# Kernel tuning notes

Hardware: AMD Instinct MI355X
Metric: run time of the kernel (lower is better)

## Reference

```python
import jax, jax.numpy as jnp
import numpy as np

D_MODEL = 512
NUM_HEADS = 8
HEAD_DIM = D_MODEL // NUM_HEADS
LN_EPS = 1e-5


def setup_inputs() -> dict:
    key = jax.random.key(0)
    ks = jax.random.split(key, 12)
    B, S, D = 4, 8192, D_MODEL
    scale = 1.0 / np.sqrt(D)  # xavier-ish init
    inp = {
        "x": jax.random.normal(ks[0], (B, S, D), dtype=jnp.float32),
        "Wq": jax.random.normal(ks[1], (D, D), dtype=jnp.float32) * scale,
        "bq": jnp.zeros((D,), dtype=jnp.float32),
        "Wk": jax.random.normal(ks[2], (D, D), dtype=jnp.float32) * scale,
        "bk": jnp.zeros((D,), dtype=jnp.float32),
        "Wv": jax.random.normal(ks[3], (D, D), dtype=jnp.float32) * scale,
        "bv": jnp.zeros((D,), dtype=jnp.float32),
        "Wo": jax.random.normal(ks[4], (D, D), dtype=jnp.float32) * scale,
        "bo": jnp.zeros((D,), dtype=jnp.float32),
        "gamma": jnp.ones((D,), dtype=jnp.float32),
        "beta": jnp.zeros((D,), dtype=jnp.float32),
    }
    return inp


def _split_heads(t, B, S):
    # (B, S, D) -> (B, H, S, hd)
    return t.reshape(B, S, NUM_HEADS, HEAD_DIM).transpose(0, 2, 1, 3)


def _feature_map(t):
    return jax.nn.elu(t) + 1.0


def reference(x, Wq, bq, Wk, bk, Wv, bv, Wo, bo, gamma, beta):
    B, S, D = x.shape
    q = _split_heads(x @ Wq + bq, B, S)
    k = _split_heads(x @ Wk + bk, B, S)
    v = _split_heads(x @ Wv + bv, B, S)

    q = _feature_map(q)
    k = _feature_map(k)

    # kv summary: (B, H, hd, hd) -- O(n d^2) instead of O(n^2 d)
    kv = jnp.einsum('bhnd,bhnm->bhdm', k, v)
    out = jnp.einsum('bhnd,bhdm->bhnm', q, kv)

    k_sum = k.sum(axis=2)  # (B, H, hd)
    normalizer = jnp.clip(jnp.einsum('bhnd,bhd->bhn', q, k_sum), 1e-6, None)
    out = out / normalizer[..., None]

    # merge heads: (B, H, S, hd) -> (B, S, D)
    out = out.transpose(0, 2, 1, 3).reshape(B, S, D)
    out = out @ Wo + bo

    # residual + layer norm (dropout is identity in eval / p=0)
    y = x + out
    mean = y.mean(axis=-1, keepdims=True)
    var = y.var(axis=-1, keepdims=True)
    y = (y - mean) * jax.lax.rsqrt(var + LN_EPS)
    return y * gamma + beta
```

## Files before the change

kernel.cpp:

```cpp
#include <hip/hip_runtime.h>
#include <cstdint>

#define SEQ     8192
#define BATCH   4
#define NHEAD   8
#define NTOK    (BATCH*SEQ)

typedef __bf16 bf16x8 __attribute__((ext_vector_type(8)));
typedef float  floatx4 __attribute__((ext_vector_type(4)));

static __device__ __forceinline__ float b2f(uint16_t h) {
    return __uint_as_float(((uint32_t)h) << 16);
}
static __device__ __forceinline__ uint16_t f2b(float f) {
    uint32_t u = __float_as_uint(f);
    u += 0x7fffu + ((u >> 16) & 1u);
    return (uint16_t)(u >> 16);
}

static __device__ __forceinline__ void async_copy16(const uint16_t* g, uint16_t* l) {
#if __has_builtin(__builtin_amdgcn_global_load_lds)
    __builtin_amdgcn_global_load_lds(
        (const __attribute__((address_space(1))) void*)g,
        (__attribute__((address_space(3))) void*)l, 16, 0, 0);
#else
    *(uint4*)l = *(const uint4*)g;
#endif
}

__global__ __launch_bounds__(256) void convert_x(
    const float* __restrict__ X, uint16_t* __restrict__ Xb)
{
    const size_t i = ((size_t)blockIdx.x * 256 + threadIdx.x) * 8;
    float4 f0 = *(const float4*)(X + i);
    float4 f1 = *(const float4*)(X + i + 4);
    uint4 o;
    uint16_t* p = (uint16_t*)&o;
    p[0]=f2b(f0.x); p[1]=f2b(f0.y); p[2]=f2b(f0.z); p[3]=f2b(f0.w);
    p[4]=f2b(f1.x); p[5]=f2b(f1.y); p[6]=f2b(f1.z); p[7]=f2b(f1.w);
    *(uint4*)(Xb + i) = o;
}

__global__ __launch_bounds__(256) void convert_w(
    const float* __restrict__ Wq, const float* __restrict__ Wk,
    const float* __restrict__ Wv, const float* __restrict__ Wo,
    uint16_t* __restrict__ out)
{
    const int z = blockIdx.z;
    const float* W = (z == 0) ? Wq : (z == 1) ? Wk : (z == 2) ? Wv : Wo;
    uint16_t* o = out + (size_t)z * 262144;
    const int n0 = blockIdx.x * 64, k0 = blockIdx.y * 64;
    __shared__ uint16_t tl[64][64];
    const int t = threadIdx.x;
    const int r  = t >> 4;
    const int c4 = (t & 15) * 4;
    #pragma unroll
    for (int s = 0; s < 4; ++s) {
        const int k = r + s * 16;
        float4 f = *(const float4*)(W + (size_t)(k0 + k) * 512 + n0 + c4);
        tl[c4 + 0][k] = f2b(f.x); tl[c4 + 1][k] = f2b(f.y);
        tl[c4 + 2][k] = f2b(f.z); tl[c4 + 3][k] = f2b(f.w);
    }
    __syncthreads();
    const int n  = t >> 2;
    const int kk = (t & 3) * 16;
    uint4* dst = (uint4*)(o + (size_t)(n0 + n) * 512 + k0 + kk);
    dst[0] = *(const uint4*)&tl[n][kk];
    dst[1] = *(const uint4*)&tl[n][kk + 8];
}

__global__ __launch_bounds__(256) void qkv128(
    const uint16_t* __restrict__ Xb,
    const uint16_t* __restrict__ Wt,
    const float* __restrict__ bq_, const float* __restrict__ bk_,
    const float* __restrict__ bv_,
    uint16_t* __restrict__ outQ, uint16_t* __restrict__ outK,
    uint16_t* __restrict__ outV)
{
    const int id = blockIdx.x;
    const int c  = id & 7;
    const int r_ = id >> 3;
    const int j_ = r_ % 12;
    const int s  = (r_ / 12) * 8 + c;
    const int proj = j_ >> 2;
    const int n0   = (j_ & 3) * 128;
    const int m0   = s * 128;

    const uint16_t* W = Wt + (size_t)proj * 262144;
    const float* bias = (proj == 0) ? bq_ : (proj == 1) ? bk_ : bv_;
    uint16_t* out     = (proj == 0) ? outQ : (proj == 1) ? outK : outV;
    const int act = (proj < 2);

    __shared__ uint16_t smem[16384];
    const int t = threadIdx.x;
    const int wave = t >> 6, lane = t & 63, quad = lane >> 4, lrow = lane & 15;
    const int wm = (wave & 1) * 64, wn = (wave >> 1) * 64;
    const int sr = t >> 2;
    const int sc = (t & 3) * 8;

    const uint16_t* gA = Xb + (size_t)(m0 + sr) * 512 + sc;
    const uint16_t* gB = W  + (size_t)(n0 + sr) * 512 + sc;

    floatx4 acc[4][4] = {};

    async_copy16(gA,            smem + t * 8);
    async_copy16(gA + 64 * 512, smem + (t + 256) * 8);
    async_copy16(gB,            smem + 4096 + t * 8);
    async_copy16(gB + 64 * 512, smem + 4096 + (t + 256) * 8);
    __syncthreads();

    int cur = 0;
    for (int k0 = 0; k0 < 512; k0 += 32) {
        const int nxt = cur ^ 1;
        if (k0 + 32 < 512) {
            const uint16_t* pA = gA + k0 + 32;
            async_copy16(pA,            smem + nxt * 8192 + t * 8);
            async_copy16(pA + 64 * 512, smem + nxt * 8192 + (t + 256) * 8);
            const uint16_t* pB = gB + k0 + 32;
            async_copy16(pB,            smem + nxt * 8192 + 4096 + t * 8);
            async_copy16(pB + 64 * 512, smem + nxt * 8192 + 4096 + (t + 256) * 8);
        }
        const uint16_t* base = smem + cur * 8192;
        bf16x8 af[4], bfr[4];
        #pragma unroll
        for (int i = 0; i < 4; ++i)
            af[i] = *(const bf16x8*)(base + (wm + i * 16 + lrow) * 32 + quad * 8);
        #pragma unroll
        for (int j = 0; j < 4; ++j)
            bfr[j] = *(const bf16x8*)(base + 4096 + (wn + j * 16 + lrow) * 32 + quad * 8);
        #pragma unroll
        for (int i = 0; i < 4; ++i)
            #pragma unroll
            for (int j = 0; j < 4; ++j)
                acc[i][j] = __builtin_amdgcn_mfma_f32_16x16x32_bf16(af[i], bfr[j], acc[i][j], 0, 0, 0);
        __syncthreads();
        cur = nxt;
    }

    #pragma unroll
    for (int j = 0; j < 4; ++j) {
        const int col = wn + j * 16 + lrow;
        const float bb = bias[n0 + col];
        #pragma unroll
        for (int i = 0; i < 4; ++i) {
            #pragma unroll
            for (int r = 0; r < 4; ++r) {
                const int row = wm + i * 16 + quad * 4 + r;
                float v = acc[i][j][r] + bb;
                if (act) v = (v > 0.0f) ? (v + 1.0f) : __expf(v);
                smem[row * 128 + (col ^ (((row >> 2) & 3) << 4))] = f2b(v);
            }
        }
    }
    __syncthreads();
    #pragma unroll
    for (int p = 0; p < 8; ++p) {
        const int idx = p * 256 + t;
        const int row = idx >> 4;
        const int cc  = (idx & 15) * 8;
        uint4 v = *(const uint4*)(smem + row * 128 + (cc ^ (((row >> 2) & 3) << 4)));
        *(uint4*)(out + (size_t)(m0 + row) * 512 + n0 + cc) = v;
    }
}

__global__ __launch_bounds__(256) void gemm_out128(
    const uint16_t* __restrict__ A,
    const uint16_t* __restrict__ Wt,
    const float* __restrict__ bias,
    const float* __restrict__ resid,
    uint16_t* __restrict__ out)
{
    const int id = blockIdx.x;
    const int c  = id & 7;
    const int r_ = id >> 3;
    const int j_ = r_ & 3;
    const int s  = (r_ >> 2) * 8 + c;
    const int n0 = j_ * 128;
    const int m0 = s * 128;

    __shared__ uint16_t smem[16384];
    const int t = threadIdx.x;
    const int wave = t >> 6, lane = t & 63, quad = lane >> 4, lrow = lane & 15;
    const int wm = (wave & 1) * 64, wn = (wave >> 1) * 64;
    const int sr = t >> 2;
    const int sc = (t & 3) * 8;

    const uint16_t* gA = A  + (size_t)(m0 + sr) * 512 + sc;
    const uint16_t* gB = Wt + (size_t)(n0 + sr) * 512 + sc;

    floatx4 acc[4][4] = {};

    async_copy16(gA,            smem + t * 8);
    async_copy16(gA + 64 * 512, smem + (t + 256) * 8);
    async_copy16(gB,            smem + 4096 + t * 8);
    async_copy16(gB + 64 * 512, smem + 4096 + (t + 256) * 8);
    __syncthreads();

    int cur = 0;
    for (int k0 = 0; k0 < 512; k0 += 32) {
        const int nxt = cur ^ 1;
        if (k0 + 32 < 512) {
            const uint16_t* pA = gA + k0 + 32;
            async_copy16(pA,            smem + nxt * 8192 + t * 8);
            async_copy16(pA + 64 * 512, smem + nxt * 8192 + (t + 256) * 8);
            const uint16_t* pB = gB + k0 + 32;
            async_copy16(pB,            smem + nxt * 8192 + 4096 + t * 8);
            async_copy16(pB + 64 * 512, smem + nxt * 8192 + 4096 + (t + 256) * 8);
        }
        const uint16_t* base = smem + cur * 8192;
        bf16x8 af[4], bfr[4];
        #pragma unroll
        for (int i = 0; i < 4; ++i)
            af[i] = *(const bf16x8*)(base + (wm + i * 16 + lrow) * 32 + quad * 8);
        #pragma unroll
        for (int j = 0; j < 4; ++j)
            bfr[j] = *(const bf16x8*)(base + 4096 + (wn + j * 16 + lrow) * 32 + quad * 8);
        #pragma unroll
        for (int i = 0; i < 4; ++i)
            #pragma unroll
            for (int j = 0; j < 4; ++j)
                acc[i][j] = __builtin_amdgcn_mfma_f32_16x16x32_bf16(af[i], bfr[j], acc[i][j], 0, 0, 0);
        __syncthreads();
        cur = nxt;
    }

    #pragma unroll
    for (int j = 0; j < 4; ++j) {
        const int col = wn + j * 16 + lrow;
        const float bb = bias[n0 + col];
        #pragma unroll
        for (int i = 0; i < 4; ++i) {
            #pragma unroll
            for (int r = 0; r < 4; ++r) {
                const int row = wm + i * 16 + quad * 4 + r;
                float v = acc[i][j][r] + bb
                        + resid[(size_t)(m0 + row) * 512 + n0 + col];
                smem[row * 128 + (col ^ (((row >> 2) & 3) << 4))] = f2b(v);
            }
        }
    }
    __syncthreads();
    #pragma unroll
    for (int p = 0; p < 8; ++p) {
        const int idx = p * 256 + t;
        const int row = idx >> 4;
        const int cc  = (idx & 15) * 8;
        uint4 v = *(const uint4*)(smem + row * 128 + (cc ^ (((row >> 2) & 3) << 4)));
        *(uint4*)(out + (size_t)(m0 + row) * 512 + n0 + cc) = v;
    }
}

__global__ __launch_bounds__(256) void kv_accum(
    const uint16_t* __restrict__ K,
    const uint16_t* __restrict__ V,
    float* __restrict__ KV,
    float* __restrict__ KSUM)
{
    const int chunk = blockIdx.x;
    const int h     = blockIdx.y;
    const int b     = blockIdx.z;
    const int t    = threadIdx.x;
    const int wv   = t >> 6;
    const int lane = t & 63;
    const int quad = lane >> 4;
    const int lrow = lane & 15;

    __shared__ uint16_t kt[64 * 66];
    __shared__ uint16_t vt[64 * 66];

    floatx4 acc[4] = {};
    floatx4 accS = {};
    union { uint16_t u[8]; bf16x8 v; } one_u;
    #pragma unroll
    for (int j = 0; j < 8; ++j) one_u.u[j] = 0x3F80;
    const bf16x8 ones = one_u.v;

    const size_t base = ((size_t)(b * SEQ + chunk * 512)) * 512 + h * 64;

    for (int n0 = 0; n0 < 512; n0 += 64) {
        #pragma unroll
        for (int s = 0; s < 2; ++s) {
            const int i   = t + 256 * s;
            const int tok = i >> 3;
            const int d0  = (i & 7) * 8;
            uint4 kq = *(const uint4*)(K + base + (size_t)(n0 + tok) * 512 + d0);
            const uint16_t* kp = (const uint16_t*)&kq;
            #pragma unroll
            for (int j = 0; j < 8; ++j) kt[(d0 + j) * 66 + tok] = kp[j];
            uint4 vq = *(const uint4*)(V + base + (size_t)(n0 + tok) * 512 + d0);
            const uint16_t* vp = (const uint16_t*)&vq;
            #pragma unroll
            for (int j = 0; j < 8; ++j) vt[(d0 + j) * 66 + tok] = vp[j];
        }
        __syncthreads();
        #pragma unroll
        for (int ks = 0; ks < 2; ++ks) {
            bf16x8 af = *(const bf16x8*)(kt + (wv * 16 + lrow) * 66 + ks * 32 + quad * 8);
            accS = __builtin_amdgcn_mfma_f32_16x16x32_bf16(af, ones, accS, 0, 0, 0);
            #pragma unroll
            for (int nt = 0; nt < 4; ++nt) {
                bf16x8 bf = *(const bf16x8*)(vt + (nt * 16 + lrow) * 66 + ks * 32 + quad * 8);
                acc[nt] = __builtin_amdgcn_mfma_f32_16x16x32_bf16(af, bf, acc[nt], 0, 0, 0);
            }
        }
        __syncthreads();
    }

    float* kvp = KV + (size_t)(b * NHEAD + h) * 4096;
    #pragma unroll
    for (int nt = 0; nt < 4; ++nt) {
        const int m = nt * 16 + lrow;
        #pragma unroll
        for (int r = 0; r < 4; ++r) {
            const int d = wv * 16 + quad * 4 + r;
            atomicAdd(kvp + d * 64 + m, acc[nt][r]);
        }
    }
    if (lrow == 0) {
        float* kp = KSUM + (size_t)(b * NHEAD + h) * 64;
        #pragma unroll
        for (int r = 0; r < 4; ++r)
            atomicAdd(kp + wv * 16 + quad * 4 + r, accS[r]);
    }
}

__global__ __launch_bounds__(256) void attn_apply(
    const uint16_t* __restrict__ Q,
    const float* __restrict__ KVg,
    const float* __restrict__ KSg,
    uint16_t* __restrict__ OUT)
{
    const int h    = blockIdx.y;
    const int tok0 = blockIdx.x * 64;
    const int b    = tok0 >> 13;
    const int t    = threadIdx.x;
    const int wv   = t >> 6;
    const int lane = t & 63;
    const int quad = lane >> 4;
    const int lrow = lane & 15;

    __shared__ uint16_t bt[64 * 66];
    __shared__ uint16_t ksb[64];

    const float* kvp = KVg + (size_t)(b * NHEAD + h) * 4096;
    #pragma unroll
    for (int s = 0; s < 16; ++s) {
        const int e = t + 256 * s;
        const int d = e >> 6, m = e & 63;
        bt[m * 66 + d] = f2b(kvp[e]);
    }
    if (t < 64) ksb[t] = f2b(KSg[(size_t)(b * NHEAD + h) * 64 + t]);
    __syncthreads();

    floatx4 acc[4] = {};
    floatx4 accN = {};
    const uint16_t* qrow = Q + (size_t)(tok0 + wv * 16 + lrow) * 512 + h * 64 + quad * 8;
    #pragma unroll
    for (int ks = 0; ks < 2; ++ks) {
        bf16x8 af = *(const bf16x8*)(qrow + ks * 32);
        bf16x8 bks = *(const bf16x8*)(ksb + ks * 32 + quad * 8);
        accN = __builtin_amdgcn_mfma_f32_16x16x32_bf16(af, bks, accN, 0, 0, 0);
        #pragma unroll
        for (int nt = 0; nt < 4; ++nt) {
            bf16x8 bf = *(const bf16x8*)(bt + (nt * 16 + lrow) * 66 + ks * 32 + quad * 8);
            acc[nt] = __builtin_amdgcn_mfma_f32_16x16x32_bf16(af, bf, acc[nt], 0, 0, 0);
        }
    }

    __syncthreads();
    #pragma unroll
    for (int r = 0; r < 4; ++r) {
        const float inv = 1.0f / fmaxf(accN[r], 1e-6f);
        const int row = wv * 16 + quad * 4 + r;
        #pragma unroll
        for (int nt = 0; nt < 4; ++nt) {
            const int col = nt * 16 + lrow;
            bt[row * 64 + (col ^ (((row >> 2) & 3) << 4))] = f2b(acc[nt][r] * inv);
        }
    }
    __syncthreads();
    #pragma unroll
    for (int p = 0; p < 2; ++p) {
        const int idx = p * 256 + t;
        const int row = idx >> 3;
        const int cc  = (idx & 7) * 8;
        uint4 v = *(const uint4*)(bt + row * 64 + (cc ^ (((row >> 2) & 3) << 4)));
        *(uint4*)(OUT + (size_t)(tok0 + row) * 512 + h * 64 + cc) = v;
    }
}

__global__ __launch_bounds__(256) void ln_rows(
    const uint16_t* __restrict__ Z,
    const float* __restrict__ gamma,
    const float* __restrict__ beta,
    float* __restrict__ OUT)
{
    const int t = threadIdx.x;
    const int wv = t >> 6, lane = t & 63;
    const size_t row = (size_t)blockIdx.x * 4 + wv;
    union { uint4 q; uint16_t u[8]; } zz;
    zz.q = *(const uint4*)(Z + row * 512 + lane * 8);
    float v[8], s = 0.f, s2 = 0.f;
    #pragma unroll
    for (int j = 0; j < 8; ++j) {
        v[j] = b2f(zz.u[j]);
        s += v[j]; s2 += v[j] * v[j];
    }
    #pragma unroll
    for (int off = 32; off > 0; off >>= 1) {
        s  += __shfl_xor(s, off, 64);
        s2 += __shfl_xor(s2, off, 64);
    }
    const float mean = s * (1.0f / 512.0f);
    const float var  = s2 * (1.0f / 512.0f) - mean * mean;
    const float inv  = rsqrtf(var + 1e-5f);
    float4 g0 = *(const float4*)(gamma + lane * 8);
    float4 g1 = *(const float4*)(gamma + lane * 8 + 4);
    float4 b0 = *(const float4*)(beta + lane * 8);
    float4 b1 = *(const float4*)(beta + lane * 8 + 4);
    float4 o0, o1;
    o0.x = (v[0]-mean)*inv*g0.x + b0.x;  o0.y = (v[1]-mean)*inv*g0.y + b0.y;
    o0.z = (v[2]-mean)*inv*g0.z + b0.z;  o0.w = (v[3]-mean)*inv*g0.w + b0.w;
    o1.x = (v[4]-mean)*inv*g1.x + b1.x;  o1.y = (v[5]-mean)*inv*g1.y + b1.y;
    o1.z = (v[6]-mean)*inv*g1.z + b1.z;  o1.w = (v[7]-mean)*inv*g1.w + b1.w;
    *(float4*)(OUT + row * 512 + lane * 8)     = o0;
    *(float4*)(OUT + row * 512 + lane * 8 + 4) = o1;
}

extern "C" void kernel_launch(void* const* d_in, const int* in_sizes, int n_in,
                              void* d_out, int out_size, void* d_ws, size_t ws_size,
                              hipStream_t stream)
{
    (void)in_sizes; (void)n_in; (void)out_size; (void)ws_size;
    const float* x     = (const float*)d_in[0];
    const float* Wq    = (const float*)d_in[1];
    const float* bq    = (const float*)d_in[2];
    const float* Wk    = (const float*)d_in[3];
    const float* bk    = (const float*)d_in[4];
    const float* Wv    = (const float*)d_in[5];
    const float* bv    = (const float*)d_in[6];
    const float* Wo    = (const float*)d_in[7];
    const float* bo    = (const float*)d_in[8];
    const float* gamma = (const float*)d_in[9];
    const float* beta  = (const float*)d_in[10];

    uint8_t* ws = (uint8_t*)d_ws;
    float*    KV   = (float*)ws;
    float*    KSUM = (float*)(ws + (size_t)32 * 4096 * 4);
    uint16_t* Wt   = (uint16_t*)(ws + (size_t)32 * 4096 * 4 + 32 * 64 * 4);
    uint16_t* phiQ = (uint16_t*)(ws + (size_t)32 * 4096 * 4 + 32 * 64 * 4
                                    + (size_t)4 * 262144 * 2);
    uint16_t* Xb   = phiQ + (size_t)NTOK * 512;
    uint16_t* phiK = (uint16_t*)d_out;
    uint16_t* vbuf = (uint16_t*)d_out + (size_t)NTOK * 512;
    uint16_t* attn = Xb;
    uint16_t* zbuf = phiQ;

    hipMemsetAsync(ws, 0, (size_t)32 * 4096 * 4 + 32 * 64 * 4, stream);

    dim3 blk(256);
    convert_x<<<dim3(NTOK * 512 / (256 * 8)), blk, 0, stream>>>(x, Xb);
    convert_w<<<dim3(8, 8, 4), blk, 0, stream>>>(Wq, Wk, Wv, Wo, Wt);
    qkv128<<<dim3(3072), blk, 0, stream>>>(
        Xb, Wt, bq, bk, bv, phiQ, phiK, vbuf);
    kv_accum<<<dim3(16, NHEAD, BATCH), blk, 0, stream>>>(phiK, vbuf, KV, KSUM);
    attn_apply<<<dim3(NTOK / 64, NHEAD), blk, 0, stream>>>(phiQ, KV, KSUM, attn);
    gemm_out128<<<dim3(1024), blk, 0, stream>>>(
        attn, Wt + (size_t)3 * 262144, bo, x, zbuf);
    ln_rows<<<dim3(NTOK / 4), blk, 0, stream>>>(zbuf, gamma, beta, (float*)d_out);
}
```

Baseline: 274.6 us.

## Triple-buffer QKV GEMM K-loop with explicit vmcnt waits

Replaces the double-buffered async global-to-LDS loop in the QKV projection GEMM with a three-stage ring buffer. Two stages are prefetched ahead, and explicit s_waitcnt vmcnt counts replace the full syncthreads waits, so loads for later K-tiles overlap with MFMA compute on the current tile. The cost is 50% more LDS per block, which may reduce occupancy, plus hand-tuned wait counts that depend on the exact number of outstanding loads.

```diff
diff --git a/kernel.cpp b/kernel.cpp
--- a/kernel.cpp
+++ b/kernel.cpp
@@ -91,7 +91,7 @@
     uint16_t* out     = (proj == 0) ? outQ : (proj == 1) ? outK : outV;
     const int act = (proj < 2);
 
-    __shared__ uint16_t smem[16384];
+    __shared__ uint16_t smem[24576];
     const int t = threadIdx.x;
     const int wave = t >> 6, lane = t & 63, quad = lane >> 4, lrow = lane & 15;
     const int wm = (wave & 1) * 64, wn = (wave >> 1) * 64;
@@ -103,24 +103,17 @@
 
     floatx4 acc[4][4] = {};
 
-    async_copy16(gA,            smem + t * 8);
-    async_copy16(gA + 64 * 512, smem + (t + 256) * 8);
-    async_copy16(gB,            smem + 4096 + t * 8);
-    async_copy16(gB + 64 * 512, smem + 4096 + (t + 256) * 8);
-    __syncthreads();
-
-    int cur = 0;
-    for (int k0 = 0; k0 < 512; k0 += 32) {
-        const int nxt = cur ^ 1;
-        if (k0 + 32 < 512) {
-            const uint16_t* pA = gA + k0 + 32;
-            async_copy16(pA,            smem + nxt * 8192 + t * 8);
-            async_copy16(pA + 64 * 512, smem + nxt * 8192 + (t + 256) * 8);
-            const uint16_t* pB = gB + k0 + 32;
-            async_copy16(pB,            smem + nxt * 8192 + 4096 + t * 8);
-            async_copy16(pB + 64 * 512, smem + nxt * 8192 + 4096 + (t + 256) * 8);
-        }
-        const uint16_t* base = smem + cur * 8192;
+    auto STAGE = [&](int st, int bi) {
+        const uint16_t* pA = gA + st * 32;
+        uint16_t* d = smem + bi * 8192;
+        async_copy16(pA,            d + t * 8);
+        async_copy16(pA + 64 * 512, d + (t + 256) * 8);
+        const uint16_t* pB = gB + st * 32;
+        async_copy16(pB,            d + 4096 + t * 8);
+        async_copy16(pB + 64 * 512, d + 4096 + (t + 256) * 8);
+    };
+    auto COMPUTE = [&](int bi) {
+        const uint16_t* base = smem + bi * 8192;
         bf16x8 af[4], bfr[4];
         #pragma unroll
         for (int i = 0; i < 4; ++i)
@@ -133,9 +126,32 @@
             #pragma unroll
             for (int j = 0; j < 4; ++j)
                 acc[i][j] = __builtin_amdgcn_mfma_f32_16x16x32_bf16(af[i], bfr[j], acc[i][j], 0, 0, 0);
-        __syncthreads();
-        cur = nxt;
-    }
+    };
+
+    STAGE(0, 0);
+    STAGE(1, 1);
+
+    int cb = 0, sb = 2;
+    for (int i = 0; i < 14; ++i) {
+        STAGE(i + 2, sb);
+        asm volatile("s_waitcnt vmcnt(8)" ::: "memory");
+        __builtin_amdgcn_s_barrier();
+        __builtin_amdgcn_sched_barrier(0);
+        COMPUTE(cb);
+        __builtin_amdgcn_s_barrier();
+        cb = (cb == 2) ? 0 : cb + 1;
+        sb = (sb == 2) ? 0 : sb + 1;
+    }
+    asm volatile("s_waitcnt vmcnt(4)" ::: "memory");
+    __builtin_amdgcn_s_barrier();
+    __builtin_amdgcn_sched_barrier(0);
+    COMPUTE(cb);
+    __builtin_amdgcn_s_barrier();
+    asm volatile("s_waitcnt vmcnt(0)" ::: "memory");
+    __builtin_amdgcn_s_barrier();
+    __builtin_amdgcn_sched_barrier(0);
+    COMPUTE(0);
+    __syncthreads();
 
     #pragma unroll
     for (int j = 0; j < 4; ++j) {
```

Result: no change. 275.9 us (+0.5%).
